# Kernel tuning notes

Hardware: AMD Instinct MI355X
Metric: run time of the kernel (lower is better)

Reference implementation:

```python
import jax, jax.numpy as jnp
import numpy as np

K = 10  # value-iteration steps


def _conv(x, w):
    # NCHW x OIHW -> NCHW, stride 1, SAME padding (pad=2 for 5x5, pad=0 for 1x1)
    return jax.lax.conv_general_dilated(
        x, w, window_strides=(1, 1), padding='SAME',
        dimension_numbers=('NCHW', 'OIHW', 'NCHW'))


def setup_inputs() -> dict:
    key = jax.random.key(0)
    ks = jax.random.split(key, 6)
    B, H, W = 64, 64, 64
    dim_h, n_hat, n_act = 150, 8, 4
    maze = jax.random.randint(ks[0], (B, H, W), 0, 3)
    # fixed embedding table from the torch module
    emb = jnp.array([[0.0, 0.0], [1.0, 0.0], [0.0, 10.0]], dtype=jnp.float32)
    encode_w = jax.random.normal(ks[1], (dim_h, 2, 5, 5), dtype=jnp.float32) * 0.05
    encode_b = jnp.zeros((dim_h,), dtype=jnp.float32)
    r_w = jax.random.normal(ks[2], (1, dim_h, 1, 1), dtype=jnp.float32) * 0.05
    q_w = jax.random.normal(ks[3], (n_hat, 1, 5, 5), dtype=jnp.float32) * 0.05
    # torch inits self.w to zeros; use small randn so the recurrence is non-trivial
    w = jax.random.normal(ks[4], (n_hat, 1, 5, 5), dtype=jnp.float32) * 0.05
    fc_w = jax.random.normal(ks[5], (n_act, n_hat), dtype=jnp.float32) * 0.1
    return dict(maze=maze, emb=emb, encode_w=encode_w, encode_b=encode_b,
                r_w=r_w, q_w=q_w, w=w, fc_w=fc_w)


def reference(maze, emb, encode_w, encode_b, r_w, q_w, w, fc_w):
    # embed: [B,H,W] -> [B,H,W,2] -> [B,2,H,W]
    m = emb[maze].transpose(0, 3, 1, 2)
    h = _conv(m, encode_w) + encode_b[None, :, None, None]  # [B,150,H,W]
    r = _conv(h, r_w)                                        # [B,1,H,W]
    q = _conv(r, q_w)                                        # [B,8,H,W]
    wk = jnp.concatenate([q_w, w], axis=1)                   # [8,2,5,5]

    def step(q, _):
        v = jnp.max(q, axis=1, keepdims=True)                # [B,1,H,W]
        q = _conv(jnp.concatenate([r, v], axis=1), wk)       # [B,8,H,W]
        return q, None

    q, _ = jax.lax.scan(step, q, None, length=K)
    q = q.transpose(0, 2, 3, 1)                              # [B,H,W,8]
    return q @ fc_w.T                                        # [B,H,W,4]
```

## Files before the change

kernel.cpp:

```cpp
#include <hip/hip_runtime.h>
#include <hip/hip_bf16.h>


#define NHAT 8
#define DIMH 150

typedef float v2f __attribute__((ext_vector_type(2)));

__global__ __launch_bounds__(512) void rq_kernel(
    const int* __restrict__ maze, const float* __restrict__ emb,
    const float* __restrict__ encode_w, const float* __restrict__ encode_b,
    const float* __restrict__ r_w, const float* __restrict__ q_w,
    float* __restrict__ q0g) {
  __shared__ float wpart[5][50];
  __shared__ float bpart[152];
  __shared__ float weff[2][25];
  __shared__ float Ts[4][25];
  __shared__ float bsh;
  __shared__ v2f qw2[25][4];
  __shared__ unsigned char mzt[24][68];
  __shared__ float rt[20][68];

  int tid = threadIdx.x;
  int b = blockIdx.y, A0 = blockIdx.x * 16;

  if (tid < 100) {
    int k = tid >> 2, j = tid & 3;
    qw2[k][j] = (v2f){q_w[(2 * j) * 25 + k], q_w[(2 * j + 1) * 25 + k]};
  }
  if (tid >= 256 && tid < 506) {
    int t2 = tid - 256;
    int chunk = t2 / 50, ik = t2 % 50;
    int i = ik / 25, k = ik % 25;
    int c0 = chunk * 30;
    float s = 0.f;
    for (int c = c0; c < c0 + 30; ++c)
      s += r_w[c] * encode_w[c * 50 + i * 25 + k];
    wpart[chunk][ik] = s;
  }
  if (tid >= 100 && tid < 250) {
    int c = tid - 100;
    bpart[c] = r_w[c] * encode_b[c];
  }
  for (int i = tid; i < 24 * 68; i += 512) {
    int mr = i / 68, mc = i % 68;
    int gy = A0 - 4 + mr, gx = mc - 2;
    unsigned char v = 3;
    if (gy >= 0 && gy < 64 && gx >= 0 && gx < 64)
      v = (unsigned char)maze[(b * 64 + gy) * 64 + gx];
    mzt[mr][mc] = v;
  }
  __syncthreads();
  if (tid < 50) {
    float s = 0.f;
#pragma unroll
    for (int ch = 0; ch < 5; ++ch) s += wpart[ch][tid];
    weff[tid / 25][tid % 25] = s;
  }
  if (tid == 50) {
    float s = 0.f;
    for (int c = 0; c < 150; ++c) s += bpart[c];
    bsh = s;
  }
  __syncthreads();
  if (tid < 100) {
    int val = tid / 25, k = tid % 25;
    float t = 0.f;
    if (val < 3) t = weff[0][k] * emb[val * 2] + weff[1][k] * emb[val * 2 + 1];
    Ts[val][k] = t;
  }
  __syncthreads();
  for (int i = tid; i < 20 * 68; i += 512) {
    int rr = i / 68, cc = i % 68;
    int gy = A0 - 2 + rr, gx = cc - 2;
    float v = 0.f;
    if (gy >= 0 && gy < 64 && gx >= 0 && gx < 64) {
      v = bsh;
#pragma unroll
      for (int ky = 0; ky < 5; ++ky)
#pragma unroll
        for (int kx = 0; kx < 5; ++kx)
          v += Ts[mzt[rr + ky][cc - 2 + kx]][ky * 5 + kx];
    }
    rt[rr][cc] = v;
  }
  __syncthreads();
  for (int i = tid; i < 16 * 64; i += 512) {
    int ly = i >> 6, gx = i & 63;
    int gy = A0 + ly;
    v2f acc[4];
#pragma unroll
    for (int j = 0; j < 4; ++j) acc[j] = (v2f){0.f, 0.f};
#pragma unroll
    for (int ky = 0; ky < 5; ++ky)
#pragma unroll
      for (int kx = 0; kx < 5; ++kx) {
        int k = ky * 5 + kx;
        float vv = rt[ly + ky][gx + kx];
        v2f vv2 = (v2f){vv, vv};
#pragma unroll
        for (int j = 0; j < 4; ++j) acc[j] += qw2[k][j] * vv2;
      }
    size_t base = ((size_t)(b * 64 + gy) * 2) * 64 + gx;
    *(float4*)&q0g[(base)*4] = make_float4(acc[0].x, acc[0].y, acc[1].x, acc[1].y);
    *(float4*)&q0g[(base + 64) * 4] =
        make_float4(acc[2].x, acc[2].y, acc[3].x, acc[3].y);
  }
}

__global__ __launch_bounds__(512, 2) void vi_kernel(
    const float* __restrict__ q0g, const float* __restrict__ w,
    const float* __restrict__ fc_w, float* __restrict__ out) {
  __shared__ __align__(16) float vbuf[2][60][68];
  __shared__ __align__(16) float tmp[52][2][64];
  __shared__ v2f wl2[25][4];

  int tid = threadIdx.x;
  int b = blockIdx.y, a0 = blockIdx.x * 16;
  int wave = tid >> 6, lane = tid & 63;
  int half = wave & 1, slot = wave >> 1;
  int roff = lane >> 4, i4 = (lane & 15) * 4;

  if (tid < 100) {
    int k = tid >> 2, j = tid & 3;
    wl2[k][j] = (v2f){w[(2 * j) * 25 + k], w[(2 * j + 1) * 25 + k]};
  }
  for (int i = tid; i < 2 * 60 * 68; i += 512) ((float*)vbuf)[i] = 0.f;
  __syncthreads();

  v2f wr0[25], wr1[25];
#pragma unroll
  for (int k = 0; k < 25; ++k) {
    wr0[k] = wl2[k][2 * half];
    wr1[k] = wl2[k][2 * half + 1];
  }

  const float* q0b = q0g + (size_t)b * 64 * 2 * 64 * 4;
  int cur = 0;

  {
    int s = max(0, a0 - 20), e = min(64, a0 + 36);
    int gx = lane;
    for (int r = s + wave; r < e; r += 8) {
      float4 f0 = *(const float4*)&q0b[(((size_t)r * 2 + 0) * 64 + gx) * 4];
      float4 f1 = *(const float4*)&q0b[(((size_t)r * 2 + 1) * 64 + gx) * 4];
      float m = fmaxf(fmaxf(fmaxf(f0.x, f0.y), fmaxf(f0.z, f0.w)),
                      fmaxf(fmaxf(f1.x, f1.y), fmaxf(f1.z, f1.w)));
      vbuf[0][r - a0 + 22][gx + 2] = m;
    }
  }
  __syncthreads();

  for (int t = 1; t <= 9; ++t) {
    int hh = 2 * (10 - t);
    int s = max(0, a0 - hh), e = min(64, a0 + 16 + hh);
    for (int rb = s + 4 * slot; rb < e; rb += 16) {
      int r = rb + roff;
      if (r < e) {
        int lr = r - a0 + 22;
        const float4* qp =
            (const float4*)&q0b[(((size_t)r * 2 + half) * 64 + i4) * 4];
        float4 qv0 = qp[0], qv1 = qp[1], qv2 = qp[2], qv3 = qp[3];
        v2f aA[4], aB[4];
        aA[0] = (v2f){qv0.x, qv0.y}; aB[0] = (v2f){qv0.z, qv0.w};
        aA[1] = (v2f){qv1.x, qv1.y}; aB[1] = (v2f){qv1.z, qv1.w};
        aA[2] = (v2f){qv2.x, qv2.y}; aB[2] = (v2f){qv2.z, qv2.w};
        aA[3] = (v2f){qv3.x, qv3.y}; aB[3] = (v2f){qv3.z, qv3.w};
#pragma unroll
        for (int jj = 0; jj < 5; ++jj) {
          const float* row = &vbuf[cur][lr - 2 + jj][i4];
          float4 fa = *(const float4*)row;
          float4 fb = *(const float4*)(row + 4);
          float f[8] = {fa.x, fa.y, fa.z, fa.w, fb.x, fb.y, fb.z, fb.w};
#pragma unroll
          for (int kx = 0; kx < 5; ++kx) {
            int k = jj * 5 + kx;
            v2f w0 = wr0[k], w1 = wr1[k];
#pragma unroll
            for (int j = 0; j < 4; ++j) {
              v2f vv2 = (v2f){f[j + kx], f[j + kx]};
              aA[j] += w0 * vv2;
              aB[j] += w1 * vv2;
            }
          }
        }
        float m0 = fmaxf(fmaxf(aA[0].x, aA[0].y), fmaxf(aB[0].x, aB[0].y));
        float m1 = fmaxf(fmaxf(aA[1].x, aA[1].y), fmaxf(aB[1].x, aB[1].y));
        float m2 = fmaxf(fmaxf(aA[2].x, aA[2].y), fmaxf(aB[2].x, aB[2].y));
        float m3 = fmaxf(fmaxf(aA[3].x, aA[3].y), fmaxf(aB[3].x, aB[3].y));
        *(float4*)&tmp[lr - 4][half][i4] = make_float4(m0, m1, m2, m3);
      }
    }
    __syncthreads();
    int n = e - s;
    for (int idx = tid; idx < n * 64; idx += 512) {
      int rr = idx >> 6, px = idx & 63;
      int lr2 = s - a0 + 22 + rr;
      vbuf[cur ^ 1][lr2][px + 2] =
          fmaxf(tmp[lr2 - 4][0][px], tmp[lr2 - 4][1][px]);
    }
    __syncthreads();
    cur ^= 1;
  }

  float fcp[4][4];
#pragma unroll
  for (int a = 0; a < 4; ++a)
#pragma unroll
    for (int cc = 0; cc < 4; ++cc) fcp[a][cc] = fc_w[a * 8 + 4 * half + cc];
  float* ptmp = (float*)tmp;

  {
    int r = a0 + 4 * slot + roff;
    int lr = r - a0 + 22;
    const float4* qp =
        (const float4*)&q0b[(((size_t)r * 2 + half) * 64 + i4) * 4];
    float4 qv0 = qp[0], qv1 = qp[1], qv2 = qp[2], qv3 = qp[3];
    v2f aA[4], aB[4];
    aA[0] = (v2f){qv0.x, qv0.y}; aB[0] = (v2f){qv0.z, qv0.w};
    aA[1] = (v2f){qv1.x, qv1.y}; aB[1] = (v2f){qv1.z, qv1.w};
    aA[2] = (v2f){qv2.x, qv2.y}; aB[2] = (v2f){qv2.z, qv2.w};
    aA[3] = (v2f){qv3.x, qv3.y}; aB[3] = (v2f){qv3.z, qv3.w};
#pragma unroll
    for (int jj = 0; jj < 5; ++jj) {
      const float* row = &vbuf[cur][lr - 2 + jj][i4];
      float4 fa = *(const float4*)row;
      float4 fb = *(const float4*)(row + 4);
      float f[8] = {fa.x, fa.y, fa.z, fa.w, fb.x, fb.y, fb.z, fb.w};
#pragma unroll
      for (int kx = 0; kx < 5; ++kx) {
        int k = jj * 5 + kx;
        v2f w0 = wr0[k], w1 = wr1[k];
#pragma unroll
        for (int j = 0; j < 4; ++j) {
          v2f vv2 = (v2f){f[j + kx], f[j + kx]};
          aA[j] += w0 * vv2;
          aB[j] += w1 * vv2;
        }
      }
    }
    float4 pp[4];
#pragma unroll
    for (int j = 0; j < 4; ++j) {
      float q0v = aA[j].x, q1v = aA[j].y, q2v = aB[j].x, q3v = aB[j].y;
      pp[j].x = fcp[0][0] * q0v + fcp[0][1] * q1v + fcp[0][2] * q2v + fcp[0][3] * q3v;
      pp[j].y = fcp[1][0] * q0v + fcp[1][1] * q1v + fcp[1][2] * q2v + fcp[1][3] * q3v;
      pp[j].z = fcp[2][0] * q0v + fcp[2][1] * q1v + fcp[2][2] * q2v + fcp[2][3] * q3v;
      pp[j].w = fcp[3][0] * q0v + fcp[3][1] * q1v + fcp[3][2] * q2v + fcp[3][3] * q3v;
    }
    if (half == 1) {
#pragma unroll
      for (int j = 0; j < 4; ++j)
        *(float4*)&ptmp[(((r - a0) * 64) + i4 + j) * 4] = pp[j];
    }
    __syncthreads();
    if (half == 0) {
#pragma unroll
      for (int j = 0; j < 4; ++j) {
        float4 o = *(const float4*)&ptmp[(((r - a0) * 64) + i4 + j) * 4];
        o.x += pp[j].x; o.y += pp[j].y; o.z += pp[j].z; o.w += pp[j].w;
        *(float4*)&out[((size_t)((b * 64 + r) * 64 + i4 + j)) * 4] = o;
      }
    }
  }
}

extern "C" void kernel_launch(void* const* d_in, const int* in_sizes, int n_in,
                              void* d_out, int out_size, void* d_ws, size_t ws_size,
                              hipStream_t stream) {
  const int* maze = (const int*)d_in[0];
  const float* emb = (const float*)d_in[1];
  const float* encode_w = (const float*)d_in[2];
  const float* encode_b = (const float*)d_in[3];
  const float* r_w = (const float*)d_in[4];
  const float* q_w = (const float*)d_in[5];
  const float* w = (const float*)d_in[6];
  const float* fc_w = (const float*)d_in[7];
  float* out = (float*)d_out;

  float* q0g = (float*)d_ws;

  rq_kernel<<<dim3(4, 64), 512, 0, stream>>>(maze, emb, encode_w, encode_b,
                                             r_w, q_w, q0g);
  vi_kernel<<<dim3(4, 64), 512, 0, stream>>>(q0g, w, fc_w, out);
}
```

Baseline: 114.5 us.

## Fuse half-channel max into stencil reads, removing combine pass and barrier

Each half writes its partial channel-max straight into a double-buffered [row][half][col] LDS layout. The final max over the two halves is now taken when the 5x5 stencil reads its neighbourhood, instead of in a separate combine loop. This removes one __syncthreads and one LDS pass per value-iteration step. In exchange each stencil row needs twice as many LDS float4 loads plus extra fmax work, and the output stores are now scalar and offset by 2, so they are unaligned.

```diff
diff --git a/kernel.cpp b/kernel.cpp
--- a/kernel.cpp
+++ b/kernel.cpp
@@ -111,8 +111,7 @@
 __global__ __launch_bounds__(512, 2) void vi_kernel(
     const float* __restrict__ q0g, const float* __restrict__ w,
     const float* __restrict__ fc_w, float* __restrict__ out) {
-  __shared__ __align__(16) float vbuf[2][60][68];
-  __shared__ __align__(16) float tmp[52][2][64];
+  __shared__ __align__(16) float tbuf[2][56][2][68];
   __shared__ v2f wl2[25][4];
 
   int tid = threadIdx.x;
@@ -125,7 +124,7 @@
     int k = tid >> 2, j = tid & 3;
     wl2[k][j] = (v2f){w[(2 * j) * 25 + k], w[(2 * j + 1) * 25 + k]};
   }
-  for (int i = tid; i < 2 * 60 * 68; i += 512) ((float*)vbuf)[i] = 0.f;
+  for (int i = tid; i < 2 * 56 * 2 * 68; i += 512) ((float*)tbuf)[i] = 0.f;
   __syncthreads();
 
   v2f wr0[25], wr1[25];
@@ -146,7 +145,9 @@
       float4 f1 = *(const float4*)&q0b[(((size_t)r * 2 + 1) * 64 + gx) * 4];
       float m = fmaxf(fmaxf(fmaxf(f0.x, f0.y), fmaxf(f0.z, f0.w)),
                       fmaxf(fmaxf(f1.x, f1.y), fmaxf(f1.z, f1.w)));
-      vbuf[0][r - a0 + 22][gx + 2] = m;
+      int lr = r - a0 + 20;
+      tbuf[0][lr][0][gx + 2] = m;
+      tbuf[0][lr][1][gx + 2] = m;
     }
   }
   __syncthreads();
@@ -157,7 +158,7 @@
     for (int rb = s + 4 * slot; rb < e; rb += 16) {
       int r = rb + roff;
       if (r < e) {
-        int lr = r - a0 + 22;
+        int lr = r - a0 + 20;
         const float4* qp =
             (const float4*)&q0b[(((size_t)r * 2 + half) * 64 + i4) * 4];
         float4 qv0 = qp[0], qv1 = qp[1], qv2 = qp[2], qv3 = qp[3];
@@ -168,10 +169,16 @@
         aA[3] = (v2f){qv3.x, qv3.y}; aB[3] = (v2f){qv3.z, qv3.w};
 #pragma unroll
         for (int jj = 0; jj < 5; ++jj) {
-          const float* row = &vbuf[cur][lr - 2 + jj][i4];
-          float4 fa = *(const float4*)row;
-          float4 fb = *(const float4*)(row + 4);
-          float f[8] = {fa.x, fa.y, fa.z, fa.w, fb.x, fb.y, fb.z, fb.w};
+          const float* r0p = &tbuf[cur][lr - 2 + jj][0][i4];
+          const float* r1p = &tbuf[cur][lr - 2 + jj][1][i4];
+          float4 ha = *(const float4*)r0p;
+          float4 hb = *(const float4*)(r0p + 4);
+          float4 ka = *(const float4*)r1p;
+          float4 kb = *(const float4*)(r1p + 4);
+          float f[8] = {fmaxf(ha.x, ka.x), fmaxf(ha.y, ka.y),
+                        fmaxf(ha.z, ka.z), fmaxf(ha.w, ka.w),
+                        fmaxf(hb.x, kb.x), fmaxf(hb.y, kb.y),
+                        fmaxf(hb.z, kb.z), fmaxf(hb.w, kb.w)};
 #pragma unroll
           for (int kx = 0; kx < 5; ++kx) {
             int k = jj * 5 + kx;
@@ -188,16 +195,9 @@
         float m1 = fmaxf(fmaxf(aA[1].x, aA[1].y), fmaxf(aB[1].x, aB[1].y));
         float m2 = fmaxf(fmaxf(aA[2].x, aA[2].y), fmaxf(aB[2].x, aB[2].y));
         float m3 = fmaxf(fmaxf(aA[3].x, aA[3].y), fmaxf(aB[3].x, aB[3].y));
-        *(float4*)&tmp[lr - 4][half][i4] = make_float4(m0, m1, m2, m3);
-      }
-    }
-    __syncthreads();
-    int n = e - s;
-    for (int idx = tid; idx < n * 64; idx += 512) {
-      int rr = idx >> 6, px = idx & 63;
-      int lr2 = s - a0 + 22 + rr;
-      vbuf[cur ^ 1][lr2][px + 2] =
-          fmaxf(tmp[lr2 - 4][0][px], tmp[lr2 - 4][1][px]);
+        float* dst = &tbuf[cur ^ 1][lr][half][i4 + 2];
+        dst[0] = m0; dst[1] = m1; dst[2] = m2; dst[3] = m3;
+      }
     }
     __syncthreads();
     cur ^= 1;
@@ -208,11 +208,11 @@
   for (int a = 0; a < 4; ++a)
 #pragma unroll
     for (int cc = 0; cc < 4; ++cc) fcp[a][cc] = fc_w[a * 8 + 4 * half + cc];
-  float* ptmp = (float*)tmp;
+  float* ptmp = (float*)&tbuf[cur ^ 1][0][0][0];
 
   {
     int r = a0 + 4 * slot + roff;
-    int lr = r - a0 + 22;
+    int lr = r - a0 + 20;
     const float4* qp =
         (const float4*)&q0b[(((size_t)r * 2 + half) * 64 + i4) * 4];
     float4 qv0 = qp[0], qv1 = qp[1], qv2 = qp[2], qv3 = qp[3];
@@ -223,10 +223,16 @@
     aA[3] = (v2f){qv3.x, qv3.y}; aB[3] = (v2f){qv3.z, qv3.w};
 #pragma unroll
     for (int jj = 0; jj < 5; ++jj) {
-      const float* row = &vbuf[cur][lr - 2 + jj][i4];
-      float4 fa = *(const float4*)row;
-      float4 fb = *(const float4*)(row + 4);
-      float f[8] = {fa.x, fa.y, fa.z, fa.w, fb.x, fb.y, fb.z, fb.w};
+      const float* r0p = &tbuf[cur][lr - 2 + jj][0][i4];
+      const float* r1p = &tbuf[cur][lr - 2 + jj][1][i4];
+      float4 ha = *(const float4*)r0p;
+      float4 hb = *(const float4*)(r0p + 4);
+      float4 ka = *(const float4*)r1p;
+      float4 kb = *(const float4*)(r1p + 4);
+      float f[8] = {fmaxf(ha.x, ka.x), fmaxf(ha.y, ka.y),
+                    fmaxf(ha.z, ka.z), fmaxf(ha.w, ka.w),
+                    fmaxf(hb.x, kb.x), fmaxf(hb.y, kb.y),
+                    fmaxf(hb.z, kb.z), fmaxf(hb.w, kb.w)};
 #pragma unroll
       for (int kx = 0; kx < 5; ++kx) {
         int k = jj * 5 + kx;
@@ -248,6 +254,7 @@
       pp[j].z = fcp[2][0] * q0v + fcp[2][1] * q1v + fcp[2][2] * q2v + fcp[2][3] * q3v;
       pp[j].w = fcp[3][0] * q0v + fcp[3][1] * q1v + fcp[3][2] * q2v + fcp[3][3] * q3v;
     }
+    __syncthreads();
     if (half == 1) {
 #pragma unroll
       for (int j = 0; j < 4; ++j)
```

Measured after the change: 119.3 us. +4.2%, slower.
